# Performance work log

Hardware: AMD Instinct MI355X
Metric: run time of the kernel (lower is better)

Reference implementation:

```python
import jax, jax.numpy as jnp
import numpy as np

N_SRC = 1024     # source frames
N_TGT = 100000   # target pool frames
D = 1024         # WavLM layer-6 feature dim
K = 4            # neighbors


def setup_inputs() -> dict:
    key = jax.random.key(0)
    k1, k2 = jax.random.split(key)
    source_feats = jax.random.normal(k1, (N_SRC, D), dtype=jnp.float32)
    target_feats = jax.random.normal(k2, (N_TGT, D), dtype=jnp.float32)
    return {"source_feats": source_feats, "target_feats": target_feats, "k": K}


def reference(source_feats, target_feats, k):
    # Cosine distance kNN: smallest cosine distance == largest cosine similarity.
    s = source_feats / jnp.linalg.norm(source_feats, axis=-1, keepdims=True)
    t = target_feats / jnp.linalg.norm(target_feats, axis=-1, keepdims=True)
    sim = jnp.einsum('nd,md->nm', s, t)          # [N_SRC, N_TGT]
    _, idx = jax.lax.top_k(sim, k)               # [N_SRC, k] neighbor indices
    # Gather ORIGINAL (un-normalized) target rows and average over neighbors,
    # matching sklearn kneighbors + target_np[indices].mean(axis=0).
    gathered = target_feats[idx]                 # [N_SRC, k, D]
    return gathered.mean(axis=1)                 # [N_SRC, D]
```

## Files before the change

### kernel.cpp

```cpp
#include <hip/hip_runtime.h>
#include <hip/hip_bf16.h>
#include <float.h>

#define N_SRC 1024
#define N_TGT 100000
#define DIM   1024
#define KNN   4

#define BM 128
#define BN 256
#define BK 32
#define NKT (DIM / BK)
#define NMB 782
#define N_TGT2 (NMB * BM)
#define NSC (N_SRC / BN)
#define NBLK (NMB * NSC)
#define NSTRIP NMB
#define NCAND (NSTRIP * KNN)
#define RERANK 16

#define SRC_KT_B 65536ull
#define TGT_KT_B ((unsigned long long)N_TGT2 * 64ull)

typedef __attribute__((ext_vector_type(8))) short bf16x8;
typedef __attribute__((ext_vector_type(4))) float f32x4;
typedef __attribute__((ext_vector_type(4))) unsigned int u32x4;

__device__ __forceinline__ unsigned int pack_trunc(float a, float b) {
    return __builtin_amdgcn_perm(__builtin_bit_cast(unsigned int, b),
                                 __builtin_bit_cast(unsigned int, a),
                                 0x07060302u);
}

__device__ __forceinline__ void gload16(const void* gp, void* lp) {
    __builtin_amdgcn_global_load_lds(
        (const __attribute__((address_space(1))) void*)gp,
        (__attribute__((address_space(3))) void*)lp, 16, 0, 0);
}

__device__ __forceinline__ void ce_desc(float& v1, int& i1, float& v2, int& i2)
{
    bool sw = (v2 > v1) || (v2 == v1 && i2 < i1);
    float tv = sw ? v2 : v1; float uv = sw ? v1 : v2;
    int   ti = sw ? i2 : i1; int   ui = sw ? i1 : i2;
    v1 = tv; i1 = ti; v2 = uv; i2 = ui;
}

__global__ __launch_bounds__(256) void convert_src_kernel(
    const float* __restrict__ src, unsigned int* __restrict__ srcws)
{
    int gid  = blockIdx.x * 256 + threadIdx.x;
    int ks   = gid >> 12;
    int rem  = gid & 4095;
    int row  = rem >> 2;
    int slot = rem & 3;
    int kin  = ks * BK + ((slot ^ ((row >> 1) & 3)) << 3);
    const float4* p = (const float4*)(src + (size_t)row * DIM + kin);
    float4 a = p[0], b = p[1];
    u32x4 o = { pack_trunc(a.x, a.y), pack_trunc(a.z, a.w),
                pack_trunc(b.x, b.y), pack_trunc(b.z, b.w) };
    ((u32x4*)srcws)[gid] = o;
}

__global__ __launch_bounds__(256) void prep_tgt_kernel(
    const float* __restrict__ tgt, unsigned int* __restrict__ tgtbf,
    float* __restrict__ invnw)
{
    __shared__ float pn[32][9];
    const int t   = threadIdx.x;
    const int r8  = t & 7;
    const int kt  = t >> 3;
    const int row = blockIdx.x * 8 + r8;
    const bool valid = row < N_TGT;

    float4 v[8];
    if (valid) {
        const float4* p = (const float4*)(tgt + (size_t)row * DIM + kt * BK);
        #pragma unroll
        for (int i = 0; i < 8; ++i) v[i] = p[i];
    } else {
        #pragma unroll
        for (int i = 0; i < 8; ++i) v[i] = make_float4(0.f, 0.f, 0.f, 0.f);
    }
    float nsq = 0.f;
    #pragma unroll
    for (int i = 0; i < 8; ++i)
        nsq += v[i].x * v[i].x + v[i].y * v[i].y
             + v[i].z * v[i].z + v[i].w * v[i].w;

    u32x4* o = (u32x4*)((char*)tgtbf + (size_t)kt * TGT_KT_B
                        + (size_t)row * 64);
    const int f = (row >> 1) & 3;
    #pragma unroll
    for (int c = 0; c < 4; ++c) {
        float4 a = v[2 * c], b2 = v[2 * c + 1];
        o[c ^ f] = (u32x4){ pack_trunc(a.x, a.y), pack_trunc(a.z, a.w),
                            pack_trunc(b2.x, b2.y), pack_trunc(b2.z, b2.w) };
    }

    pn[kt][r8] = nsq;
    __syncthreads();
    if (t < 8) {
        float s = 0.f;
        #pragma unroll
        for (int k = 0; k < 32; ++k) s += pn[k][t];
        int r2 = blockIdx.x * 8 + t;
        invnw[r2] = (r2 < N_TGT) ? 1.0f / sqrtf(s) : -1.0f;
    }
}

__global__ __launch_bounds__(512, 4) void gemm_topk_bf_kernel(
    const void* __restrict__ tgtbf, const void* __restrict__ srcbf,
    const float* __restrict__ invnw,
    float* __restrict__ cand_val, int* __restrict__ cand_idx)
{
    __shared__ __align__(16) unsigned short As[2][BM][BK];
    __shared__ __align__(16) unsigned short Bs[2][BN][BK];
    __shared__ float invn_sh[BM];
    __shared__ float scv[2 * BN * KNN];
    __shared__ int   sci[2 * BN * KNN];

    const int b = blockIdx.x;
    const int logical = (b & 7) * (NBLK / 8) + (b >> 3);
    const int mblk = logical >> 2;
    const int schk = logical & 3;
    const int m0 = mblk * BM;
    const int c0 = schk * BN;

    const int t = threadIdx.x;
    const int lane = t & 63;
    const int w = t >> 6;
    const int wm = w >> 2, wn = w & 3;
    const int g = lane >> 4, li = lane & 15;

    const char* tb_ = (const char*)tgtbf;
    const char* sb_ = (const char*)srcbf;

    f32x4 acc[4][4];
    #pragma unroll
    for (int i = 0; i < 4; ++i)
        #pragma unroll
        for (int j = 0; j < 4; ++j) acc[i][j] = (f32x4){0.f, 0.f, 0.f, 0.f};

    unsigned short *Ac = &As[0][0][0], *An = &As[1][0][0];
    unsigned short *Bc = &Bs[0][0][0], *Bn = &Bs[1][0][0];

    #define STAGE(Ab_, Bb_, kt_) do {                                         \
        const char* ga_ = tb_ + (size_t)(kt_) * TGT_KT_B + (size_t)m0 * 64    \
                          + (size_t)t * 16;                                   \
        gload16(ga_, (Ab_) + t * 8);                                          \
        const char* gb_ = sb_ + (size_t)(kt_) * SRC_KT_B + (size_t)c0 * 64    \
                          + (size_t)t * 16;                                   \
        gload16(gb_,        (Bb_) + t * 8);                                   \
        gload16(gb_ + 8192, (Bb_) + 4096 + t * 8);                            \
    } while (0)

    const int sl = (g ^ ((li >> 1) & 3)) * 8;

    #define READ_AB do {                                                      \
        _Pragma("unroll")                                                     \
        for (int mf = 0; mf < 4; ++mf)                                        \
            af[mf] = *(const bf16x8*)(Ac + (wm * 64 + mf * 16 + li) * BK + sl);\
        _Pragma("unroll")                                                     \
        for (int nf = 0; nf < 4; ++nf)                                        \
            bf[nf] = *(const bf16x8*)(Bc + (wn * 64 + nf * 16 + li) * BK + sl);\
    } while (0)

    #define DO_MFMA do {                                                      \
        _Pragma("unroll")                                                     \
        for (int mf = 0; mf < 4; ++mf)                                        \
            _Pragma("unroll")                                                 \
            for (int nf = 0; nf < 4; ++nf)                                    \
                acc[mf][nf] = __builtin_amdgcn_mfma_f32_16x16x32_bf16(        \
                    af[mf], bf[nf], acc[mf][nf], 0, 0, 0);                    \
    } while (0)

    STAGE(Ac, Bc, 0);
    __syncthreads();

    for (int kt = 0; kt < NKT; ++kt) {
        if (kt + 1 < NKT) STAGE(An, Bn, kt + 1);
        bf16x8 af[4], bf[4];
        READ_AB;
        DO_MFMA;
        __syncthreads();
        unsigned short* tmp_;
        tmp_ = Ac; Ac = An; An = tmp_;
        tmp_ = Bc; Bc = Bn; Bn = tmp_;
    }
    #undef STAGE
    #undef READ_AB
    #undef DO_MFMA

    if (t < BM) invn_sh[t] = invnw[m0 + t];
    __syncthreads();

    float invr[4][4];
    #pragma unroll
    for (int mf = 0; mf < 4; ++mf)
        #pragma unroll
        for (int j = 0; j < 4; ++j)
            invr[mf][j] = invn_sh[wm * 64 + mf * 16 + g * 4 + j];

    #pragma unroll
    for (int nf = 0; nf < 4; ++nf) {
        const int col = wn * 64 + nf * 16 + li;
        float s[4][4];
        #pragma unroll
        for (int mf = 0; mf < 4; ++mf)
            #pragma unroll
            for (int j = 0; j < 4; ++j)
                s[mf][j] = (invr[mf][j] > 0.f) ? acc[mf][nf][j] * invr[mf][j]
                                               : -FLT_MAX;
        #pragma unroll
        for (int it = 0; it < KNN; ++it) {
            float bv = -FLT_MAX; int bli = 0;
            #pragma unroll
            for (int mf = 0; mf < 4; ++mf)
                #pragma unroll
                for (int j = 0; j < 4; ++j) {
                    int id = mf * 16 + g * 4 + j;
                    if (s[mf][j] > bv) { bv = s[mf][j]; bli = id; }
                }
            #pragma unroll
            for (int off = 16; off < 64; off <<= 1) {
                float ov = __shfl_xor(bv, off);
                int   oi = __shfl_xor(bli, off);
                if (ov > bv || (ov == bv && oi < bli)) { bv = ov; bli = oi; }
            }
            const int mfw = bli >> 4, gw = (bli >> 2) & 3, jw = bli & 3;
            if (g == gw) {
                #pragma unroll
                for (int mf = 0; mf < 4; ++mf)
                    #pragma unroll
                    for (int j = 0; j < 4; ++j)
                        if (mf == mfw && j == jw) s[mf][j] = -FLT_MAX;
            }
            if (g == it) {
                int o = (wm * BN + col) * KNN + it;
                scv[o] = bv;
                sci[o] = m0 + wm * 64 + bli;
            }
        }
    }
    __syncthreads();

    if (t < BN) {
        float v4[4] = { -FLT_MAX, -FLT_MAX, -FLT_MAX, -FLT_MAX };
        int   i4[4] = { 0x7fffffff, 0x7fffffff, 0x7fffffff, 0x7fffffff };
        #pragma unroll
        for (int q = 0; q < 8; ++q) {
            int o = ((q >> 2) * BN + t) * KNN + (q & 3);
            float v = scv[o]; int ix = sci[o];
            if (v > v4[3] || (v == v4[3] && ix < i4[3])) {
                v4[3] = v; i4[3] = ix;
                ce_desc(v4[2], i4[2], v4[3], i4[3]);
                ce_desc(v4[1], i4[1], v4[2], i4[2]);
                ce_desc(v4[0], i4[0], v4[1], i4[1]);
            }
        }
        size_t o = ((size_t)(c0 + t) * NSTRIP + mblk) * KNN;
        #pragma unroll
        for (int it = 0; it < KNN; ++it) {
            cand_val[o + it] = v4[it];
            cand_idx[o + it] = i4[it];
        }
    }
}

__global__ __launch_bounds__(256) void merge_rerank_kernel(
    const float* __restrict__ src, const float* __restrict__ tgt,
    const float* __restrict__ cand_val, const int* __restrict__ cand_idx,
    float* __restrict__ out)
{
    __shared__ float sv[NCAND];
    __shared__ float red_v[4];
    __shared__ int   red_p[4];
    __shared__ int   topi[RERANK];
    __shared__ float rsim[RERANK];
    __shared__ int   ridx[RERANK];
    __shared__ int   sel[KNN];

    const int row = blockIdx.x;
    const int t = threadIdx.x, lane = t & 63, w = t >> 6;
    const float* cv = cand_val + (size_t)row * NCAND;
    const int*   ci = cand_idx + (size_t)row * NCAND;

    for (int i = t; i < NCAND; i += 256) sv[i] = cv[i];
    __syncthreads();

    for (int it = 0; it < RERANK; ++it) {
        float bv = -FLT_MAX; int bp = 0;
        for (int i = t; i < NCAND; i += 256) {
            float v = sv[i];
            if (v > bv) { bv = v; bp = i; }
        }
        #pragma unroll
        for (int off = 1; off < 64; off <<= 1) {
            float ov = __shfl_xor(bv, off);
            int   op = __shfl_xor(bp, off);
            if (ov > bv || (ov == bv && op < bp)) { bv = ov; bp = op; }
        }
        if (lane == 0) { red_v[w] = bv; red_p[w] = bp; }
        __syncthreads();
        if (t == 0) {
            float Bv = red_v[0]; int Bp = red_p[0];
            for (int q = 1; q < 4; ++q)
                if (red_v[q] > Bv || (red_v[q] == Bv && red_p[q] < Bp)) {
                    Bv = red_v[q]; Bp = red_p[q];
                }
            topi[it] = ci[Bp];
            sv[Bp] = -FLT_MAX;
        }
        __syncthreads();
    }

    const float4* sp = (const float4*)(src + (size_t)row * DIM);
    #pragma unroll
    for (int q = 0; q < 4; ++q) {
        int cidx = topi[w + 4 * q];
        const float4* tp = (const float4*)(tgt + (size_t)cidx * DIM);
        float a = 0.f, nn = 0.f;
        #pragma unroll
        for (int p = 0; p < 4; ++p) {
            float4 x = sp[lane + 64 * p], y = tp[lane + 64 * p];
            a  = fmaf(x.x, y.x, a);  a  = fmaf(x.y, y.y, a);
            a  = fmaf(x.z, y.z, a);  a  = fmaf(x.w, y.w, a);
            nn = fmaf(y.x, y.x, nn); nn = fmaf(y.y, y.y, nn);
            nn = fmaf(y.z, y.z, nn); nn = fmaf(y.w, y.w, nn);
        }
        #pragma unroll
        for (int off = 1; off < 64; off <<= 1) {
            a  += __shfl_xor(a, off);
            nn += __shfl_xor(nn, off);
        }
        if (lane == 0) { rsim[w + 4 * q] = a / sqrtf(nn); ridx[w + 4 * q] = cidx; }
    }
    __syncthreads();

    if (w == 0) {
        float v = (lane < RERANK) ? rsim[lane] : -FLT_MAX;
        int  ix = (lane < RERANK) ? ridx[lane] : 0x7fffffff;
        #pragma unroll
        for (int it = 0; it < KNN; ++it) {
            float bv = v; int bix = ix;
            #pragma unroll
            for (int off = 1; off < 16; off <<= 1) {
                float ov = __shfl_xor(bv, off);
                int   oi = __shfl_xor(bix, off);
                if (ov > bv || (ov == bv && oi < bix)) { bv = ov; bix = oi; }
            }
            if (lane == 0) sel[it] = bix;
            if (ix == bix) v = -FLT_MAX;
        }
    }
    __syncthreads();

    const float4* g0 = (const float4*)(tgt + (size_t)sel[0] * DIM);
    const float4* g1 = (const float4*)(tgt + (size_t)sel[1] * DIM);
    const float4* g2 = (const float4*)(tgt + (size_t)sel[2] * DIM);
    const float4* g3 = (const float4*)(tgt + (size_t)sel[3] * DIM);
    float4* po = (float4*)(out + (size_t)row * DIM);
    float4 v0 = g0[t], v1 = g1[t], v2 = g2[t], v3 = g3[t];
    float4 rr;
    rr.x = (v0.x + v1.x + v2.x + v3.x) * 0.25f;
    rr.y = (v0.y + v1.y + v2.y + v3.y) * 0.25f;
    rr.z = (v0.z + v1.z + v2.z + v3.z) * 0.25f;
    rr.w = (v0.w + v1.w + v2.w + v3.w) * 0.25f;
    po[t] = rr;
}

extern "C" void kernel_launch(void* const* d_in, const int* in_sizes, int n_in,
                              void* d_out, int out_size, void* d_ws, size_t ws_size,
                              hipStream_t stream)
{
    const float* src = (const float*)d_in[0];
    const float* tgt = (const float*)d_in[1];
    float* out = (float*)d_out;

    const size_t SRCBF_B = 2097152;
    const size_t TGTBF_B = (size_t)N_TGT2 * 2048;
    const size_t INVN_B  = (size_t)N_TGT2 * 4;
    const size_t CV_B    = (size_t)N_SRC * NCAND * 4;

    char* p = (char*)d_ws;
    unsigned int* srcbf = (unsigned int*)p;
    unsigned int* tgtbf = (unsigned int*)(p + SRCBF_B);
    float* invnw    = (float*)(p + SRCBF_B + TGTBF_B);
    float* cand_val = (float*)(p + SRCBF_B + TGTBF_B + INVN_B);
    int*   cand_idx = (int*)(p + SRCBF_B + TGTBF_B + INVN_B + CV_B);

    convert_src_kernel<<<512, 256, 0, stream>>>(src, srcbf);
    prep_tgt_kernel<<<N_TGT2 / 8, 256, 0, stream>>>(tgt, tgtbf, invnw);
    gemm_topk_bf_kernel<<<NBLK, 512, 0, stream>>>(tgtbf, srcbf, invnw,
                                                  cand_val, cand_idx);
    merge_rerank_kernel<<<N_SRC, 256, 0, stream>>>(src, tgt,
                                                   cand_val, cand_idx, out);
}
```

Before: 462.8 us.

## Switch similarity GEMM from bf16 to fp8 MFMA and widen exact rerank

Target and source features are now quantized to fp8 (e4m3 via cvt_pk_fp8) instead of truncated bf16, with BK doubled to 64 so each 16-byte LDS load still feeds two fp8 MFMAs. This halves the packed-target workspace and the GEMM's memory traffic, and uses the higher fp8 MFMA throughput. To offset the coarser similarity approximation, the exact fp32 rerank candidate count grows from 16 to 32. Lower precision may still drop true neighbours from the approximate per-strip top-k, which could change the selected indices.

```diff
diff --git a/kernel.cpp b/kernel.cpp
--- a/kernel.cpp
+++ b/kernel.cpp
@@ -9,7 +9,7 @@
 
 #define BM 128
 #define BN 256
-#define BK 32
+#define BK 64
 #define NKT (DIM / BK)
 #define NMB 782
 #define N_TGT2 (NMB * BM)
@@ -17,20 +17,14 @@
 #define NBLK (NMB * NSC)
 #define NSTRIP NMB
 #define NCAND (NSTRIP * KNN)
-#define RERANK 16
+#define RERANK 32
 
 #define SRC_KT_B 65536ull
 #define TGT_KT_B ((unsigned long long)N_TGT2 * 64ull)
 
-typedef __attribute__((ext_vector_type(8))) short bf16x8;
 typedef __attribute__((ext_vector_type(4))) float f32x4;
 typedef __attribute__((ext_vector_type(4))) unsigned int u32x4;
-
-__device__ __forceinline__ unsigned int pack_trunc(float a, float b) {
-    return __builtin_amdgcn_perm(__builtin_bit_cast(unsigned int, b),
-                                 __builtin_bit_cast(unsigned int, a),
-                                 0x07060302u);
-}
+typedef __attribute__((ext_vector_type(2))) long long i64x2;
 
 __device__ __forceinline__ void gload16(const void* gp, void* lp) {
     __builtin_amdgcn_global_load_lds(
@@ -38,6 +32,13 @@
         (__attribute__((address_space(3))) void*)lp, 16, 0, 0);
 }
 
+__device__ __forceinline__ unsigned int pk_fp8x4(float x0, float x1,
+                                                 float x2, float x3) {
+    int d = __builtin_amdgcn_cvt_pk_fp8_f32(x0, x1, 0, false);
+    d     = __builtin_amdgcn_cvt_pk_fp8_f32(x2, x3, d, true);
+    return (unsigned int)d;
+}
+
 __device__ __forceinline__ void ce_desc(float& v1, int& i1, float& v2, int& i2)
 {
     bool sw = (v2 > v1) || (v2 == v1 && i2 < i1);
@@ -49,16 +50,19 @@
 __global__ __launch_bounds__(256) void convert_src_kernel(
     const float* __restrict__ src, unsigned int* __restrict__ srcws)
 {
-    int gid  = blockIdx.x * 256 + threadIdx.x;
-    int ks   = gid >> 12;
-    int rem  = gid & 4095;
-    int row  = rem >> 2;
-    int slot = rem & 3;
-    int kin  = ks * BK + ((slot ^ ((row >> 1) & 3)) << 3);
-    const float4* p = (const float4*)(src + (size_t)row * DIM + kin);
-    float4 a = p[0], b = p[1];
-    u32x4 o = { pack_trunc(a.x, a.y), pack_trunc(a.z, a.w),
-                pack_trunc(b.x, b.y), pack_trunc(b.z, b.w) };
+    int gid = blockIdx.x * 256 + threadIdx.x;
+    int kt  = gid >> 12;
+    int rem = gid & 4095;
+    int row = rem >> 2;
+    int pos = rem & 3;
+    int c   = pos ^ ((row >> 1) & 3);
+    const float4* p0 = (const float4*)(src + (size_t)row * DIM + kt * BK + c * 8);
+    const float4* p1 = (const float4*)(src + (size_t)row * DIM + kt * BK + 32 + c * 8);
+    float4 a0 = p0[0], a1 = p0[1], b0 = p1[0], b1 = p1[1];
+    u32x4 o = { pk_fp8x4(a0.x, a0.y, a0.z, a0.w),
+                pk_fp8x4(a1.x, a1.y, a1.z, a1.w),
+                pk_fp8x4(b0.x, b0.y, b0.z, b0.w),
+                pk_fp8x4(b1.x, b1.y, b1.z, b1.w) };
     ((u32x4*)srcws)[gid] = o;
 }
 
@@ -66,25 +70,25 @@
     const float* __restrict__ tgt, unsigned int* __restrict__ tgtbf,
     float* __restrict__ invnw)
 {
-    __shared__ float pn[32][9];
-    const int t   = threadIdx.x;
-    const int r8  = t & 7;
-    const int kt  = t >> 3;
-    const int row = blockIdx.x * 8 + r8;
+    __shared__ float pn[16][17];
+    const int t  = threadIdx.x;
+    const int li = t & 15;
+    const int kt = t >> 4;
+    const int row = blockIdx.x * 16 + li;
     const bool valid = row < N_TGT;
 
-    float4 v[8];
+    float4 v[16];
     if (valid) {
         const float4* p = (const float4*)(tgt + (size_t)row * DIM + kt * BK);
         #pragma unroll
-        for (int i = 0; i < 8; ++i) v[i] = p[i];
+        for (int i = 0; i < 16; ++i) v[i] = p[i];
     } else {
         #pragma unroll
-        for (int i = 0; i < 8; ++i) v[i] = make_float4(0.f, 0.f, 0.f, 0.f);
+        for (int i = 0; i < 16; ++i) v[i] = make_float4(0.f, 0.f, 0.f, 0.f);
     }
     float nsq = 0.f;
     #pragma unroll
-    for (int i = 0; i < 8; ++i)
+    for (int i = 0; i < 16; ++i)
         nsq += v[i].x * v[i].x + v[i].y * v[i].y
              + v[i].z * v[i].z + v[i].w * v[i].w;
 
@@ -93,29 +97,32 @@
     const int f = (row >> 1) & 3;
     #pragma unroll
     for (int c = 0; c < 4; ++c) {
-        float4 a = v[2 * c], b2 = v[2 * c + 1];
-        o[c ^ f] = (u32x4){ pack_trunc(a.x, a.y), pack_trunc(a.z, a.w),
-                            pack_trunc(b2.x, b2.y), pack_trunc(b2.z, b2.w) };
-    }
-
-    pn[kt][r8] = nsq;
-    __syncthreads();
-    if (t < 8) {
+        float4 a0 = v[2 * c], a1 = v[2 * c + 1];
+        float4 b0 = v[8 + 2 * c], b1 = v[8 + 2 * c + 1];
+        o[c ^ f] = (u32x4){ pk_fp8x4(a0.x, a0.y, a0.z, a0.w),
+                            pk_fp8x4(a1.x, a1.y, a1.z, a1.w),
+                            pk_fp8x4(b0.x, b0.y, b0.z, b0.w),
+                            pk_fp8x4(b1.x, b1.y, b1.z, b1.w) };
+    }
+
+    pn[li][kt] = nsq;
+    __syncthreads();
+    if (t < 16) {
         float s = 0.f;
         #pragma unroll
-        for (int k = 0; k < 32; ++k) s += pn[k][t];
-        int r2 = blockIdx.x * 8 + t;
+        for (int k = 0; k < 16; ++k) s += pn[t][k];
+        int r2 = blockIdx.x * 16 + t;
         invnw[r2] = (r2 < N_TGT) ? 1.0f / sqrtf(s) : -1.0f;
     }
 }
 
-__global__ __launch_bounds__(512, 4) void gemm_topk_bf_kernel(
+__global__ __launch_bounds__(512, 4) void gemm_topk_fp8_kernel(
     const void* __restrict__ tgtbf, const void* __restrict__ srcbf,
     const float* __restrict__ invnw,
     float* __restrict__ cand_val, int* __restrict__ cand_idx)
 {
-    __shared__ __align__(16) unsigned short As[2][BM][BK];
-    __shared__ __align__(16) unsigned short Bs[2][BN][BK];
+    __shared__ __align__(16) unsigned char As[2][BM][BK];
+    __shared__ __align__(16) unsigned char Bs[2][BN][BK];
     __shared__ float invn_sh[BM];
     __shared__ float scv[2 * BN * KNN];
     __shared__ int   sci[2 * BN * KNN];
@@ -142,28 +149,28 @@
         #pragma unroll
         for (int j = 0; j < 4; ++j) acc[i][j] = (f32x4){0.f, 0.f, 0.f, 0.f};
 
-    unsigned short *Ac = &As[0][0][0], *An = &As[1][0][0];
-    unsigned short *Bc = &Bs[0][0][0], *Bn = &Bs[1][0][0];
+    unsigned char *Ac = &As[0][0][0], *An = &As[1][0][0];
+    unsigned char *Bc = &Bs[0][0][0], *Bn = &Bs[1][0][0];
 
     #define STAGE(Ab_, Bb_, kt_) do {                                         \
         const char* ga_ = tb_ + (size_t)(kt_) * TGT_KT_B + (size_t)m0 * 64    \
                           + (size_t)t * 16;                                   \
-        gload16(ga_, (Ab_) + t * 8);                                          \
+        gload16(ga_, (Ab_) + t * 16);                                         \
         const char* gb_ = sb_ + (size_t)(kt_) * SRC_KT_B + (size_t)c0 * 64    \
                           + (size_t)t * 16;                                   \
-        gload16(gb_,        (Bb_) + t * 8);                                   \
-        gload16(gb_ + 8192, (Bb_) + 4096 + t * 8);                            \
+        gload16(gb_,        (Bb_) + t * 16);                                  \
+        gload16(gb_ + 8192, (Bb_) + 8192 + t * 16);                           \
     } while (0)
 
-    const int sl = (g ^ ((li >> 1) & 3)) * 8;
+    const int sl = (g ^ ((li >> 1) & 3)) * 16;
 
     #define READ_AB do {                                                      \
         _Pragma("unroll")                                                     \
         for (int mf = 0; mf < 4; ++mf)                                        \
-            af[mf] = *(const bf16x8*)(Ac + (wm * 64 + mf * 16 + li) * BK + sl);\
+            af[mf] = *(const i64x2*)(Ac + (wm * 64 + mf * 16 + li) * BK + sl);\
         _Pragma("unroll")                                                     \
         for (int nf = 0; nf < 4; ++nf)                                        \
-            bf[nf] = *(const bf16x8*)(Bc + (wn * 64 + nf * 16 + li) * BK + sl);\
+            bf[nf] = *(const i64x2*)(Bc + (wn * 64 + nf * 16 + li) * BK + sl);\
     } while (0)
 
     #define DO_MFMA do {                                                      \
@@ -171,8 +178,14 @@
         for (int mf = 0; mf < 4; ++mf)                                        \
             _Pragma("unroll")                                                 \
             for (int nf = 0; nf < 4; ++nf)                                    \
-                acc[mf][nf] = __builtin_amdgcn_mfma_f32_16x16x32_bf16(        \
-                    af[mf], bf[nf], acc[mf][nf], 0, 0, 0);                    \
+                acc[mf][nf] = __builtin_amdgcn_mfma_f32_16x16x32_fp8_fp8(     \
+                    af[mf][0], bf[nf][0], acc[mf][nf], 0, 0, 0);              \
+        _Pragma("unroll")                                                     \
+        for (int mf = 0; mf < 4; ++mf)                                        \
+            _Pragma("unroll")                                                 \
+            for (int nf = 0; nf < 4; ++nf)                                    \
+                acc[mf][nf] = __builtin_amdgcn_mfma_f32_16x16x32_fp8_fp8(     \
+                    af[mf][1], bf[nf][1], acc[mf][nf], 0, 0, 0);              \
     } while (0)
 
     STAGE(Ac, Bc, 0);
@@ -180,11 +193,11 @@
 
     for (int kt = 0; kt < NKT; ++kt) {
         if (kt + 1 < NKT) STAGE(An, Bn, kt + 1);
-        bf16x8 af[4], bf[4];
+        i64x2 af[4], bf[4];
         READ_AB;
         DO_MFMA;
         __syncthreads();
-        unsigned short* tmp_;
+        unsigned char* tmp_;
         tmp_ = Ac; Ac = An; An = tmp_;
         tmp_ = Bc; Bc = Bn; Bn = tmp_;
     }
@@ -317,7 +330,7 @@
 
     const float4* sp = (const float4*)(src + (size_t)row * DIM);
     #pragma unroll
-    for (int q = 0; q < 4; ++q) {
+    for (int q = 0; q < 8; ++q) {
         int cidx = topi[w + 4 * q];
         const float4* tp = (const float4*)(tgt + (size_t)cidx * DIM);
         float a = 0.f, nn = 0.f;
@@ -345,7 +358,7 @@
         for (int it = 0; it < KNN; ++it) {
             float bv = v; int bix = ix;
             #pragma unroll
-            for (int off = 1; off < 16; off <<= 1) {
+            for (int off = 1; off < 32; off <<= 1) {
                 float ov = __shfl_xor(bv, off);
                 int   oi = __shfl_xor(bix, off);
                 if (ov > bv || (ov == bv && oi < bix)) { bv = ov; bix = oi; }
@@ -379,7 +392,7 @@
     float* out = (float*)d_out;
 
     const size_t SRCBF_B = 2097152;
-    const size_t TGTBF_B = (size_t)N_TGT2 * 2048;
+    const size_t TGTBF_B = (size_t)N_TGT2 * 1024;
     const size_t INVN_B  = (size_t)N_TGT2 * 4;
     const size_t CV_B    = (size_t)N_SRC * NCAND * 4;
 
@@ -390,10 +403,10 @@
     float* cand_val = (float*)(p + SRCBF_B + TGTBF_B + INVN_B);
     int*   cand_idx = (int*)(p + SRCBF_B + TGTBF_B + INVN_B + CV_B);
 
-    convert_src_kernel<<<512, 256, 0, stream>>>(src, srcbf);
-    prep_tgt_kernel<<<N_TGT2 / 8, 256, 0, stream>>>(tgt, tgtbf, invnw);
-    gemm_topk_bf_kernel<<<NBLK, 512, 0, stream>>>(tgtbf, srcbf, invnw,
-                                                  cand_val, cand_idx);
+    convert_src_kernel<<<256, 256, 0, stream>>>(src, srcbf);
+    prep_tgt_kernel<<<N_TGT2 / 16, 256, 0, stream>>>(tgt, tgtbf, invnw);
+    gemm_topk_fp8_kernel<<<NBLK, 512, 0, stream>>>(tgtbf, srcbf, invnw,
+                                                   cand_val, cand_idx);
     merge_rerank_kernel<<<N_SRC, 256, 0, stream>>>(src, tgt,
                                                    cand_val, cand_idx, out);
 }
```

New measurement: 388.4 us. 1.19x faster.
